# Kernel optimization log

Measured on AMD Instinct MI355X. Metric: run time of the kernel, lower is better.

The kernel has to match this reference:

```python
import jax, jax.numpy as jnp
import numpy as np
from jax import lax

B, C, H, W = 4, 256, 64, 64
R = 4  # reduction
BN_EPS = 1e-5


def setup_inputs() -> dict:
    key = jax.random.key(0)
    ks = jax.random.split(key, 18)
    n = jax.random.normal
    return {
        "x_self": n(ks[0], (B, C, H, W), jnp.float32),
        "x_other": n(ks[1], (B, C, H, W), jnp.float32),
        "q_w": n(ks[2], (C, C), jnp.float32) * 0.05,      # self_q 1x1 conv
        "q_b": n(ks[3], (C,), jnp.float32) * 0.05,
        "kv_w": n(ks[4], (2 * C, C), jnp.float32) * 0.05,  # other_kv 1x1 conv
        "kv_b": n(ks[5], (2 * C,), jnp.float32) * 0.05,
        "g1_w": n(ks[6], (C // R, C), jnp.float32) * 0.05,  # gate conv1
        "g1_b": n(ks[7], (C // R,), jnp.float32) * 0.05,
        "g2_w": n(ks[8], (1, C // R), jnp.float32) * 0.05,  # gate conv2
        "g2_b": n(ks[9], (1,), jnp.float32) * 0.05,
        "dw_w": n(ks[10], (C, 1, 3, 3), jnp.float32) * 0.1,  # depthwise 3x3
        "dw_b": n(ks[11], (C,), jnp.float32) * 0.05,
        "bn_g": jnp.ones((C,), jnp.float32),
        "bn_b": jnp.zeros((C,), jnp.float32),
        "bn_m": n(ks[12], (C,), jnp.float32) * 0.05,
        "bn_v": jax.random.uniform(ks[13], (C,), jnp.float32, 0.5, 1.5),
        "out_w": n(ks[14], (C, C), jnp.float32) * 0.05,
        "out_b": n(ks[15], (C,), jnp.float32) * 0.05,
    }


def _conv1x1(x, w, b):
    return jnp.einsum('bchw,oc->bohw', x, w) + b[None, :, None, None]


def reference(x_self, x_other, q_w, q_b, kv_w, kv_b, g1_w, g1_b, g2_w, g2_b,
              dw_w, dw_b, bn_g, bn_b, bn_m, bn_v, out_w, out_b):
    # local branch: depthwise 3x3 conv -> BatchNorm (eval stats) -> SiLU
    y = lax.conv_general_dilated(
        x_self, dw_w, (1, 1), 'SAME',
        feature_group_count=C,
        dimension_numbers=('NCHW', 'OIHW', 'NCHW')) + dw_b[None, :, None, None]
    scale = (bn_g / jnp.sqrt(bn_v + BN_EPS))[None, :, None, None]
    y = (y - bn_m[None, :, None, None]) * scale + bn_b[None, :, None, None]
    local_feat = y * jax.nn.sigmoid(y)  # SiLU

    # cross attention over HW tokens
    q = _conv1x1(x_self, q_w, q_b).reshape(B, C, H * W)
    kv = _conv1x1(x_other, kv_w, kv_b)
    k = kv[:, :C].reshape(B, C, H * W)
    v = kv[:, C:].reshape(B, C, H * W)
    attn = jnp.einsum('bcn,bcm->bnm', q, k) / jnp.sqrt(jnp.float32(C))  # [B,HW,HW]
    attn = jax.nn.softmax(attn, axis=-1)
    attn_out = jnp.einsum('bnm,bcm->bcn', attn, v).reshape(B, C, H, W)

    # channel-squeeze gate on x_self -> scalar per sample
    p = jnp.mean(x_self, axis=(2, 3))                 # [B,C] global avg pool
    g = jax.nn.relu(p @ g1_w.T + g1_b)                # [B,C//R]
    g = jax.nn.sigmoid(g @ g2_w.T + g2_b)             # [B,1]
    gate = g[:, :, None, None]

    fused = local_feat + gate * attn_out
    return _conv1x1(fused, out_w, out_b)
```

## Files before the change

kernel.cpp:

```cpp
#include <hip/hip_runtime.h>
#include <stdint.h>

#define BB 4
#define CC 256
#define HH 64
#define WWD 64
#define NN 4096
#define LOG2E 1.4426950408889634f

typedef __attribute__((ext_vector_type(8))) short short8;
typedef __attribute__((ext_vector_type(4))) float f32x4;
typedef __attribute__((ext_vector_type(16))) float f32x16;
typedef __attribute__((ext_vector_type(4))) unsigned short us4;
typedef unsigned long long ull;

__device__ __forceinline__ unsigned short f2bf(float f) {
  unsigned int u = __float_as_uint(f);
  u += 0x7fffu + ((u >> 16) & 1u);
  return (unsigned short)(u >> 16);
}
__device__ __forceinline__ float bf2f(unsigned short h) {
  return __uint_as_float(((unsigned int)h) << 16);
}
__device__ __forceinline__ short8 ld8(const unsigned short* p) {
  return *reinterpret_cast<const short8*>(p);
}
__device__ __forceinline__ unsigned char f2fp8(float v) {
  return (unsigned char)__builtin_amdgcn_cvt_pk_fp8_f32(v, v, 0, false);
}
__device__ __forceinline__ int rowmap(int reg, int h) {
  return (reg & 3) + 8 * (reg >> 2) + 4 * h;
}
__device__ __forceinline__ void gll16(const void* g, void* l) {
  __builtin_amdgcn_global_load_lds(
      (const __attribute__((address_space(1))) unsigned int*)g,
      (__attribute__((address_space(3))) unsigned int*)l, 16, 0, 0);
}

__global__ __launch_bounds__(256, 2) void k_pre(
    const float* __restrict__ xs, const float* __restrict__ xo,
    const float* __restrict__ dww, const float* __restrict__ dwb,
    const float* __restrict__ bng, const float* __restrict__ bnb,
    const float* __restrict__ bnm, const float* __restrict__ bnv,
    const float* __restrict__ qw, const float* __restrict__ kvw,
    const float* __restrict__ ow, unsigned short* __restrict__ XtS,
    unsigned short* __restrict__ XtO, unsigned short* __restrict__ localT,
    float* __restrict__ psumA, unsigned short* __restrict__ Wb) {
  __shared__ float rb3[3][64][67];
  __shared__ unsigned short sb[64][67];
  int tid = threadIdx.x;
  if (blockIdx.z == 8) {
    int i = (blockIdx.x * 64 + blockIdx.y) * 1024 + tid * 4;
    const float* src;
    if (i < 65536) src = qw + i;
    else if (i < 196608) src = kvw + (i - 65536);
    else src = ow + (i - 196608);
    f32x4 v = *reinterpret_cast<const f32x4*>(src);
    us4 r;
#pragma unroll
    for (int j = 0; j < 4; ++j) r[j] = f2bf(v[j]);
    *reinterpret_cast<us4*>(Wb + i) = r;
    return;
  }
  int c0 = blockIdx.x * 64, h = blockIdx.y;
  int b = blockIdx.z >> 1, which = blockIdx.z & 1;
  const float* src = which ? xo : xs;
  int wq = tid >> 6, w = tid & 63;
  int dlo = which ? 1 : 0, dhi = which ? 1 : 2;
  for (int d = dlo; d <= dhi; ++d) {
    int hh = h + d - 1;
    bool ok = (hh >= 0 && hh < HH);
#pragma unroll
    for (int p = 0; p < 4; ++p) {
      int idx = p * 256 + tid;
      int cl = idx >> 4, ws4 = (idx & 15) * 4;
      f32x4 v = {};
      if (ok)
        v = *reinterpret_cast<const f32x4*>(
            &src[(((size_t)(b * CC + c0 + cl)) * HH + hh) * WWD + ws4]);
#pragma unroll
      for (int j = 0; j < 4; ++j) rb3[d][cl][ws4 + 1 + j] = v[j];
    }
    if (tid < 64) { rb3[d][tid][0] = 0.f; rb3[d][tid][65] = 0.f; }
  }
  __syncthreads();
  unsigned short* dst = which ? XtO : XtS;
  int n0 = h * 64, cb = (tid & 15) * 4;
#pragma unroll
  for (int i = 0; i < 4; ++i) {
    int wl = i * 16 + (tid >> 4);
    us4 r;
#pragma unroll
    for (int j = 0; j < 4; ++j) r[j] = f2bf(rb3[1][cb + j][wl + 1]);
    *reinterpret_cast<us4*>(&dst[((size_t)b * NN + n0 + wl) * CC + c0 + cb]) = r;
  }
  if (which) return;
  if (tid < 64) {
    float s = 0.f;
    for (int ww = 0; ww < 64; ++ww) s += rb3[1][tid][ww + 1];
    psumA[((size_t)(b * 64 + h)) * CC + c0 + tid] = s;
  }
  for (int p = 0; p < 16; ++p) {
    int cl = p * 4 + wq, c = c0 + cl;
    float acc = 0.f;
#pragma unroll
    for (int di = 0; di < 3; ++di)
#pragma unroll
      for (int dj = 0; dj < 3; ++dj)
        acc = fmaf(rb3[di][cl][w + dj], dww[c * 9 + di * 3 + dj], acc);
    float y = acc + dwb[c];
    float sc = bng[c] * rsqrtf(bnv[c] + 1e-5f);
    float v = (y - bnm[c]) * sc + bnb[c];
    sb[cl][w] = f2bf(v / (1.f + __expf(-v)));
  }
  __syncthreads();
#pragma unroll
  for (int i = 0; i < 4; ++i) {
    int wl = i * 16 + (tid >> 4);
    us4 r;
#pragma unroll
    for (int j = 0; j < 4; ++j) r[j] = sb[cb + j][wl];
    *reinterpret_cast<us4*>(&localT[((size_t)b * NN + h * WWD + wl) * CC + c0 + cb]) = r;
  }
}

__global__ __launch_bounds__(256, 4) void k_qkv(
    const unsigned short* __restrict__ XtS, const unsigned short* __restrict__ XtO,
    const unsigned short* __restrict__ Wb, const float* __restrict__ qb,
    const float* __restrict__ kvb, const float* __restrict__ psumA,
    const float* __restrict__ g1w, const float* __restrict__ g1b,
    const float* __restrict__ g2w, const float* __restrict__ g2b,
    unsigned char* __restrict__ Qt8, unsigned char* __restrict__ Kt8,
    unsigned char* __restrict__ Vv8, float* __restrict__ gate) {
  __shared__ unsigned short Xs[64][264];
  int tid = threadIdx.x;
  int id = blockIdx.y;
  if (id == 3) {
    if (blockIdx.x != 0 || blockIdx.z != 0) return;
    float* mf = (float*)&Xs[0][0];
    float* hpf = mf + 1024;
    int c = tid;
    for (int b4 = 0; b4 < 4; ++b4) {
      float s = 0.f;
      for (int hh = 0; hh < 64; ++hh) s += psumA[((size_t)(b4 * 64 + hh)) * CC + c];
      mf[b4 * 256 + c] = s * (1.f / 4096.f);
    }
    __syncthreads();
    for (int b4 = 0; b4 < 4; ++b4) {
      int j = tid >> 2, cq = tid & 3;
      float s = 0.f;
      for (int cc = cq * 64; cc < cq * 64 + 64; ++cc)
        s = fmaf(mf[b4 * 256 + cc], g1w[j * CC + cc], s);
      hpf[j * 5 + cq] = s;
      __syncthreads();
      if (tid < 64) {
        float hh = fmaxf(hpf[tid * 5] + hpf[tid * 5 + 1] + hpf[tid * 5 + 2] +
                             hpf[tid * 5 + 3] + g1b[tid], 0.f);
        float t = hh * g2w[tid];
        for (int off = 32; off; off >>= 1) t += __shfl_down(t, off, 64);
        if (tid == 0) gate[b4] = 1.f / (1.f + expf(-(t + g2b[0])));
      }
      __syncthreads();
    }
    return;
  }
  int n0 = blockIdx.x * 64, b = blockIdx.z;
  const unsigned short* Xt = (id == 0) ? XtS : XtO;
  const unsigned short* W = Wb + id * 65536;
  int wave = tid >> 6, lane = tid & 63, l31 = lane & 31, h = lane >> 5;
#pragma unroll
  for (int p = 0; p < 8; ++p) {
    int r = p * 8 + (tid >> 5), c = (tid & 31) * 8;
    *reinterpret_cast<uint4*>(&Xs[r][c]) =
        *reinterpret_cast<const uint4*>(Xt + ((size_t)b * NN + n0 + r) * CC + c);
  }
  __syncthreads();
  int o0 = wave * 64;
  f32x16 acc[4] = {};
  if (id < 2) {
#pragma unroll
    for (int t = 0; t < 16; ++t) {
      short8 a0 = ld8(&Xs[l31][t * 16 + h * 8]);
      short8 a1 = ld8(&Xs[32 + l31][t * 16 + h * 8]);
      short8 b0 = ld8(W + (size_t)(o0 + l31) * CC + t * 16 + h * 8);
      short8 b1 = ld8(W + (size_t)(o0 + 32 + l31) * CC + t * 16 + h * 8);
      acc[0] = __builtin_amdgcn_mfma_f32_32x32x16_bf16(a0, b0, acc[0], 0, 0, 0);
      acc[1] = __builtin_amdgcn_mfma_f32_32x32x16_bf16(a0, b1, acc[1], 0, 0, 0);
      acc[2] = __builtin_amdgcn_mfma_f32_32x32x16_bf16(a1, b0, acc[2], 0, 0, 0);
      acc[3] = __builtin_amdgcn_mfma_f32_32x32x16_bf16(a1, b1, acc[3], 0, 0, 0);
    }
    const float* bias = id ? kvb : qb;
    unsigned char* Out8 = id ? Kt8 : Qt8;
    __syncthreads();
    unsigned char (*T8)[264] = reinterpret_cast<unsigned char(*)[264]>(&Xs[0][0]);
#pragma unroll
    for (int nt = 0; nt < 2; ++nt)
#pragma unroll
      for (int ot = 0; ot < 2; ++ot) {
        int o = o0 + ot * 32 + l31;
        float bv = bias[o];
#pragma unroll
        for (int reg = 0; reg < 16; ++reg) {
          int nl = nt * 32 + rowmap(reg, h);
          T8[nl][o] = f2fp8((acc[nt * 2 + ot][reg] + bv) * 0.25f);
        }
      }
    __syncthreads();
#pragma unroll
    for (int p = 0; p < 4; ++p) {
      int idx = p * 256 + tid, row = idx >> 4, cc = (idx & 15) * 16;
      int s = (id == 1) ? ((row & 31) << 3) : 0;
      ull a0 = *reinterpret_cast<const ull*>(&T8[row][cc ^ s]);
      ull a1 = *reinterpret_cast<const ull*>(&T8[row][(cc + 8) ^ s]);
      uint4 u;
      u.x = (unsigned)a0; u.y = (unsigned)(a0 >> 32);
      u.z = (unsigned)a1; u.w = (unsigned)(a1 >> 32);
      *reinterpret_cast<uint4*>(Out8 + ((size_t)b * NN + n0 + row) * CC + cc) = u;
    }
  } else {
#pragma unroll
    for (int t = 0; t < 16; ++t) {
      short8 a0 = ld8(W + (size_t)(o0 + l31) * CC + t * 16 + h * 8);
      short8 a1 = ld8(W + (size_t)(o0 + 32 + l31) * CC + t * 16 + h * 8);
      short8 b0 = ld8(&Xs[l31][t * 16 + h * 8]);
      short8 b1 = ld8(&Xs[32 + l31][t * 16 + h * 8]);
      acc[0] = __builtin_amdgcn_mfma_f32_32x32x16_bf16(a0, b0, acc[0], 0, 0, 0);
      acc[1] = __builtin_amdgcn_mfma_f32_32x32x16_bf16(a0, b1, acc[1], 0, 0, 0);
      acc[2] = __builtin_amdgcn_mfma_f32_32x32x16_bf16(a1, b0, acc[2], 0, 0, 0);
      acc[3] = __builtin_amdgcn_mfma_f32_32x32x16_bf16(a1, b1, acc[3], 0, 0, 0);
    }
    __syncthreads();
    unsigned char (*V8)[72] = reinterpret_cast<unsigned char(*)[72]>(&Xs[0][0]);
#pragma unroll
    for (int ot = 0; ot < 2; ++ot)
#pragma unroll
      for (int nt = 0; nt < 2; ++nt)
#pragma unroll
        for (int reg = 0; reg < 16; ++reg) {
          int o = o0 + ot * 32 + rowmap(reg, h);
          int nl = nt * 32 + l31;
          V8[o][nl] = f2fp8(acc[ot * 2 + nt][reg] + kvb[CC + o]);
        }
    __syncthreads();
#pragma unroll
    for (int p = 0; p < 4; ++p) {
      int idx = p * 256 + tid, o = idx >> 2, mm = (idx & 3) * 16;
      int s = (o & 7) << 3;
      ull a0 = *reinterpret_cast<const ull*>(&V8[o][mm ^ s]);
      ull a1 = *reinterpret_cast<const ull*>(&V8[o][(mm + 8) ^ s]);
      uint4 u;
      u.x = (unsigned)a0; u.y = (unsigned)(a0 >> 32);
      u.z = (unsigned)a1; u.w = (unsigned)(a1 >> 32);
      *reinterpret_cast<uint4*>(Vv8 + ((size_t)b * CC + o) * NN + n0 + mm) = u;
    }
  }
}

__global__ __launch_bounds__(256, 3) void k_flash8(
    const unsigned char* __restrict__ Qt8, const unsigned char* __restrict__ Kt8,
    const unsigned char* __restrict__ Vv8, const unsigned short* __restrict__ localT,
    const float* __restrict__ gate, unsigned short* __restrict__ Opart16,
    float* __restrict__ Lpart, unsigned short* __restrict__ fusedT) {
  __shared__ unsigned char Ks8[64][256];
  __shared__ unsigned char Vs8[2][256][64];
  __shared__ unsigned char Ps8[64][72];
  __shared__ float lred[2][64];
  int b = blockIdx.x & 3, n0 = (blockIdx.x >> 2) * 64;
  int sp = blockIdx.y, nsp = gridDim.y;
  int tid = threadIdx.x, wave = tid >> 6, lane = tid & 63, l31 = lane & 31, h = lane >> 5;
  int rw = wave & 1, cw = wave >> 1;
  int wbase = tid & ~63;
  const unsigned char* qp = Qt8 + ((size_t)b * NN + n0 + rw * 32 + l31) * CC + h * 8;
  long qf[16];
#pragma unroll
  for (int t = 0; t < 16; ++t) qf[t] = *reinterpret_cast<const long*>(qp + t * 16);
  f32x16 O[4] = {};
  float lsum = 0.f;
  int m_lo = (64 * sp) / nsp, m_hi = (64 * (sp + 1)) / nsp;
  const unsigned char* Kbase = Kt8 + (size_t)b * NN * CC;
  const unsigned char* Vbase = Vv8 + (size_t)b * CC * NN;
  {
    const unsigned char* Kg = Kbase + (size_t)(m_lo * 64) * CC;
    const unsigned char* Vg = Vbase + m_lo * 64;
    unsigned char* vdst = &Vs8[m_lo & 1][0][0];
#pragma unroll
    for (int p = 0; p < 4; ++p) {
      int idx = p * 256 + tid;
      int c = idx >> 2, mm = (idx & 3) * 16;
      gll16(Vg + (size_t)c * NN + mm, vdst + (p * 256 + wbase) * 16);
      gll16(Kg + (size_t)idx * 16, &Ks8[0][0] + (p * 256 + wbase) * 16);
    }
  }
  const unsigned char* Krow = &Ks8[cw * 32 + l31][0];
  int ksw = l31 << 3;
  int vsw = (l31 & 7) << 3;
  for (int mt = m_lo; mt < m_hi; ++mt) {
    asm volatile("s_waitcnt vmcnt(0)" ::: "memory");
    __builtin_amdgcn_s_barrier();
    __builtin_amdgcn_sched_barrier(0);
    {
      int mn = (mt + 1 < m_hi) ? mt + 1 : mt;
      const unsigned char* Vg = Vbase + mn * 64;
      unsigned char* vdst = &Vs8[(mt + 1) & 1][0][0];
#pragma unroll
      for (int p = 0; p < 4; ++p) {
        int idx = p * 256 + tid;
        int c = idx >> 2, mm = (idx & 3) * 16;
        gll16(Vg + (size_t)c * NN + mm, vdst + (p * 256 + wbase) * 16);
      }
    }
    __builtin_amdgcn_sched_barrier(0);
    f32x16 S = {};
#pragma unroll
    for (int t = 0; t < 16; ++t) {
      long kf = *reinterpret_cast<const long*>(Krow + ((t * 16 + h * 8) ^ ksw));
      S = __builtin_amdgcn_mfma_f32_32x32x16_fp8_fp8(kf, qf[t], S, 0, 0, 0);
    }
#pragma unroll
    for (int r = 0; r < 4; ++r) {
      float p0 = __builtin_exp2f(S[4 * r + 0] * LOG2E);
      float p1 = __builtin_exp2f(S[4 * r + 1] * LOG2E);
      float p2 = __builtin_exp2f(S[4 * r + 2] * LOG2E);
      float p3 = __builtin_exp2f(S[4 * r + 3] * LOG2E);
      lsum += (p0 + p1) + (p2 + p3);
      unsigned u = __builtin_amdgcn_cvt_pk_fp8_f32(p0, p1, 0, false);
      u = __builtin_amdgcn_cvt_pk_fp8_f32(p2, p3, u, true);
      *reinterpret_cast<unsigned*>(&Ps8[rw * 32 + l31][cw * 32 + 8 * r + 4 * h]) = u;
    }
    asm volatile("s_waitcnt lgkmcnt(0)" ::: "memory");
    __builtin_amdgcn_s_barrier();
    __builtin_amdgcn_sched_barrier(0);
    {
      int mn = (mt + 1 < m_hi) ? mt + 1 : mt;
      const unsigned char* Kg = Kbase + (size_t)(mn * 64) * CC;
#pragma unroll
      for (int p = 0; p < 4; ++p)
        gll16(Kg + (size_t)(p * 256 + tid) * 16, &Ks8[0][0] + (p * 256 + wbase) * 16);
    }
    __builtin_amdgcn_sched_barrier(0);
    const unsigned char (*Vc)[64] = Vs8[mt & 1];
#pragma unroll
    for (int t = 0; t < 4; ++t) {
      long pf = *reinterpret_cast<const long*>(&Ps8[rw * 32 + l31][t * 16 + h * 8]);
#pragma unroll
      for (int ct = 0; ct < 4; ++ct) {
        long vf = *reinterpret_cast<const long*>(
            &Vc[cw * 128 + ct * 32 + l31][(t * 16 + h * 8) ^ vsw]);
        O[ct] = __builtin_amdgcn_mfma_f32_32x32x16_fp8_fp8(pf, vf, O[ct], 0, 0, 0);
      }
    }
  }
  asm volatile("s_waitcnt vmcnt(0)" ::: "memory");
  lsum += __shfl_xor(lsum, 32, 64);
  __syncthreads();
  if (h == 0) lred[cw][rw * 32 + l31] = lsum;
  __syncthreads();
  size_t obase2 = (size_t)(b * nsp + sp) * NN;
  if (nsp == 1) {
    float* ltot = reinterpret_cast<float*>(&Ps8[0][0]);
    if (tid < 64) ltot[tid] = lred[0][tid] + lred[1][tid];
    __syncthreads();
    float gv = gate[b];
    float inv[16];
#pragma unroll
    for (int reg = 0; reg < 16; ++reg)
      inv[reg] = gv / ltot[rw * 32 + rowmap(reg, h)];
#pragma unroll
    for (int ct = 0; ct < 4; ++ct)
#pragma unroll
      for (int reg = 0; reg < 16; ++reg) {
        int n = n0 + rw * 32 + rowmap(reg, h);
        int c = cw * 128 + ct * 32 + l31;
        size_t idx = ((size_t)b * NN + n) * CC + c;
        fusedT[idx] = f2bf(bf2f(localT[idx]) + O[ct][reg] * inv[reg]);
      }
  } else {
    if (tid < 64) Lpart[obase2 + n0 + tid] = lred[0][tid] + lred[1][tid];
#pragma unroll
    for (int ct = 0; ct < 4; ++ct)
#pragma unroll
      for (int reg = 0; reg < 16; ++reg) {
        int n = n0 + rw * 32 + rowmap(reg, h);
        int c = cw * 128 + ct * 32 + l31;
        Opart16[(obase2 + n) * CC + c] = f2bf(O[ct][reg]);
      }
  }
}

__global__ __launch_bounds__(256, 4) void k_out(
    const unsigned short* __restrict__ W, const float* __restrict__ ob,
    const float* __restrict__ gate, const unsigned short* __restrict__ localT,
    const unsigned short* __restrict__ Opart16, const float* __restrict__ Lpart,
    const unsigned short* __restrict__ fusedT, float* __restrict__ out, int nsp) {
  __shared__ unsigned short Xs[64][264];
  int n0 = blockIdx.x * 64, o0 = blockIdx.y * 128, b = blockIdx.z;
  int tid = threadIdx.x, wave = tid >> 6, lane = tid & 63, l31 = lane & 31, h = lane >> 5;
  if (Opart16) {
    float gv = gate[b];
#pragma unroll
    for (int p = 0; p < 8; ++p) {
      int r = p * 8 + (tid >> 5), cc = (tid & 31) * 8;
      int n = n0 + r;
      float lsum = 0.f;
      for (int sp = 0; sp < nsp; ++sp) lsum += Lpart[(size_t)(b * nsp + sp) * NN + n];
      float g = gv / lsum;
      float ov[8] = {};
      for (int sp = 0; sp < nsp; ++sp) {
        short8 x = ld8(Opart16 + ((size_t)(b * nsp + sp) * NN + n) * CC + cc);
#pragma unroll
        for (int j = 0; j < 8; ++j) ov[j] += bf2f(((unsigned short*)&x)[j]);
      }
      const unsigned short* lp = localT + ((size_t)b * NN + n) * CC + cc;
      short8 lv = ld8(lp);
      us4 r0, r1;
#pragma unroll
      for (int j = 0; j < 4; ++j) {
        r0[j] = f2bf(bf2f(((unsigned short*)&lv)[j]) + ov[j] * g);
        r1[j] = f2bf(bf2f(((unsigned short*)&lv)[j + 4]) + ov[j + 4] * g);
      }
      *reinterpret_cast<us4*>(&Xs[r][cc]) = r0;
      *reinterpret_cast<us4*>(&Xs[r][cc + 4]) = r1;
    }
  } else {
#pragma unroll
    for (int p = 0; p < 8; ++p) {
      int r = p * 8 + (tid >> 5), c = (tid & 31) * 8;
      *reinterpret_cast<uint4*>(&Xs[r][c]) =
          *reinterpret_cast<const uint4*>(fusedT + ((size_t)b * NN + n0 + r) * CC + c);
    }
  }
  int obase = o0 + wave * 32;
  short8 af[16];
#pragma unroll
  for (int t = 0; t < 16; ++t) af[t] = ld8(W + (size_t)(obase + l31) * CC + t * 16 + h * 8);
  __syncthreads();
  f32x16 acc[2] = {};
#pragma unroll
  for (int t = 0; t < 16; ++t) {
    short8 b0 = ld8(&Xs[l31][t * 16 + h * 8]);
    short8 b1 = ld8(&Xs[32 + l31][t * 16 + h * 8]);
    acc[0] = __builtin_amdgcn_mfma_f32_32x32x16_bf16(af[t], b0, acc[0], 0, 0, 0);
    acc[1] = __builtin_amdgcn_mfma_f32_32x32x16_bf16(af[t], b1, acc[1], 0, 0, 0);
  }
#pragma unroll
  for (int nt = 0; nt < 2; ++nt)
#pragma unroll
    for (int reg = 0; reg < 16; ++reg) {
      int o = obase + rowmap(reg, h);
      int n = n0 + nt * 32 + l31;
      out[((size_t)b * CC + o) * NN + n] = acc[nt][reg] + ob[o];
    }
}

extern "C" void kernel_launch(void* const* d_in, const int* in_sizes, int n_in,
                              void* d_out, int out_size, void* d_ws, size_t ws_size,
                              hipStream_t stream) {
  const float* xs  = (const float*)d_in[0];
  const float* xo  = (const float*)d_in[1];
  const float* qw  = (const float*)d_in[2];
  const float* qb  = (const float*)d_in[3];
  const float* kvw = (const float*)d_in[4];
  const float* kvb = (const float*)d_in[5];
  const float* g1w = (const float*)d_in[6];
  const float* g1b = (const float*)d_in[7];
  const float* g2w = (const float*)d_in[8];
  const float* g2b = (const float*)d_in[9];
  const float* dww = (const float*)d_in[10];
  const float* dwb = (const float*)d_in[11];
  const float* bng = (const float*)d_in[12];
  const float* bnb = (const float*)d_in[13];
  const float* bnm = (const float*)d_in[14];
  const float* bnv = (const float*)d_in[15];
  const float* ow  = (const float*)d_in[16];
  const float* ob  = (const float*)d_in[17];
  float* out = (float*)d_out;
  char* ws = (char*)d_ws;

  const size_t SZ  = (size_t)BB * NN * CC * 2;
  const size_t SZ8 = (size_t)BB * NN * CC;
  unsigned short* XtS    = (unsigned short*)(ws);
  unsigned short* XtO    = (unsigned short*)(ws + SZ);
  unsigned short* localT = (unsigned short*)(ws + 2 * SZ);
  unsigned char*  Qt8    = (unsigned char*)(ws + 3 * SZ);
  unsigned char*  Kt8    = (unsigned char*)(ws + 3 * SZ + SZ8);
  unsigned char*  Vv8    = (unsigned char*)(ws + 3 * SZ + 2 * SZ8);
  unsigned short* Wb     = (unsigned short*)(ws + 3 * SZ + 3 * SZ8);
  float* psumA = (float*)(ws + 3 * SZ + 3 * SZ8 + 524288);
  float* gate  = (float*)(ws + 3 * SZ + 3 * SZ8 + 524288 + 262144);
  size_t tail  = 3 * SZ + 3 * SZ8 + 524288 + 262144 + 4096;
  float* Lpart = (float*)(ws + tail);
  unsigned short* Opart16 = (unsigned short*)(ws + tail + 262144);
  unsigned short* fusedT = XtS;

  size_t base = tail + 262144;
  int S = 1;
  if (ws_size >= base + 3ull * SZ) S = 3;
  else if (ws_size >= base + 2ull * SZ) S = 2;

  k_pre<<<dim3(4, 64, 9), 256, 0, stream>>>(xs, xo, dww, dwb, bng, bnb, bnm, bnv,
                                            qw, kvw, ow, XtS, XtO, localT, psumA, Wb);
  k_qkv<<<dim3(64, 4, 4), 256, 0, stream>>>(XtS, XtO, Wb, qb, kvb, psumA,
                                            g1w, g1b, g2w, g2b, Qt8, Kt8, Vv8, gate);
  k_flash8<<<dim3(256, S), 256, 0, stream>>>(Qt8, Kt8, Vv8, localT, gate, Opart16,
                                             Lpart, fusedT);
  k_out<<<dim3(64, 2, 4), 256, 0, stream>>>(Wb + 196608, ob, gate, localT,
                                            S > 1 ? Opart16 : nullptr, Lpart, fusedT,
                                            out, S);
}
```

Before: 258.9 us.

## Split QK MFMA chain, reuse XtO for partial output, retune V swizzle and priority

Splits the QK^T accumulation into two independent MFMA chains to shorten the dependency chain, and raises wave priority around the MFMA loops with s_setprio. Changes the V tile XOR swizzle to use row pairs, both where V is written and where it is read in the flash kernel. Stores the first split's partial output in the now-dead XtO buffer, so less extra workspace is needed and three splits become possible with smaller workspace. The risk is a mismatch between the swizzle on the write side and the read side, and extra register pressure from the second accumulator.

```diff
diff --git a/kernel.cpp b/kernel.cpp
--- a/kernel.cpp
+++ b/kernel.cpp
@@ -245,7 +245,7 @@
 #pragma unroll
     for (int p = 0; p < 4; ++p) {
       int idx = p * 256 + tid, o = idx >> 2, mm = (idx & 3) * 16;
-      int s = (o & 7) << 3;
+      int s = ((o >> 1) & 7) << 3;
       ull a0 = *reinterpret_cast<const ull*>(&V8[o][mm ^ s]);
       ull a1 = *reinterpret_cast<const ull*>(&V8[o][(mm + 8) ^ s]);
       uint4 u;
@@ -259,7 +259,8 @@
 __global__ __launch_bounds__(256, 3) void k_flash8(
     const unsigned char* __restrict__ Qt8, const unsigned char* __restrict__ Kt8,
     const unsigned char* __restrict__ Vv8, const unsigned short* __restrict__ localT,
-    const float* __restrict__ gate, unsigned short* __restrict__ Opart16,
+    const float* __restrict__ gate, unsigned short* __restrict__ OpartA,
+    unsigned short* __restrict__ OpartB,
     float* __restrict__ Lpart, unsigned short* __restrict__ fusedT) {
   __shared__ unsigned char Ks8[64][256];
   __shared__ unsigned char Vs8[2][256][64];
@@ -275,7 +276,7 @@
 #pragma unroll
   for (int t = 0; t < 16; ++t) qf[t] = *reinterpret_cast<const long*>(qp + t * 16);
   f32x16 O[4] = {};
-  float lsum = 0.f;
+  float lsumA = 0.f, lsumB = 0.f;
   int m_lo = (64 * sp) / nsp, m_hi = (64 * (sp + 1)) / nsp;
   const unsigned char* Kbase = Kt8 + (size_t)b * NN * CC;
   const unsigned char* Vbase = Vv8 + (size_t)b * CC * NN;
@@ -293,7 +294,7 @@
   }
   const unsigned char* Krow = &Ks8[cw * 32 + l31][0];
   int ksw = l31 << 3;
-  int vsw = (l31 & 7) << 3;
+  int vsw = ((l31 >> 1) & 7) << 3;
   for (int mt = m_lo; mt < m_hi; ++mt) {
     asm volatile("s_waitcnt vmcnt(0)" ::: "memory");
     __builtin_amdgcn_s_barrier();
@@ -310,19 +311,24 @@
       }
     }
     __builtin_amdgcn_sched_barrier(0);
-    f32x16 S = {};
-#pragma unroll
-    for (int t = 0; t < 16; ++t) {
-      long kf = *reinterpret_cast<const long*>(Krow + ((t * 16 + h * 8) ^ ksw));
-      S = __builtin_amdgcn_mfma_f32_32x32x16_fp8_fp8(kf, qf[t], S, 0, 0, 0);
-    }
+    f32x16 Sa = {}, Sb = {};
+    __builtin_amdgcn_s_setprio(1);
+#pragma unroll
+    for (int t = 0; t < 8; ++t) {
+      long kfa = *reinterpret_cast<const long*>(Krow + ((t * 16 + h * 8) ^ ksw));
+      long kfb = *reinterpret_cast<const long*>(Krow + (((t + 8) * 16 + h * 8) ^ ksw));
+      Sa = __builtin_amdgcn_mfma_f32_32x32x16_fp8_fp8(kfa, qf[t], Sa, 0, 0, 0);
+      Sb = __builtin_amdgcn_mfma_f32_32x32x16_fp8_fp8(kfb, qf[t + 8], Sb, 0, 0, 0);
+    }
+    __builtin_amdgcn_s_setprio(0);
 #pragma unroll
     for (int r = 0; r < 4; ++r) {
-      float p0 = __builtin_exp2f(S[4 * r + 0] * LOG2E);
-      float p1 = __builtin_exp2f(S[4 * r + 1] * LOG2E);
-      float p2 = __builtin_exp2f(S[4 * r + 2] * LOG2E);
-      float p3 = __builtin_exp2f(S[4 * r + 3] * LOG2E);
-      lsum += (p0 + p1) + (p2 + p3);
+      float p0 = __builtin_exp2f((Sa[4 * r + 0] + Sb[4 * r + 0]) * LOG2E);
+      float p1 = __builtin_exp2f((Sa[4 * r + 1] + Sb[4 * r + 1]) * LOG2E);
+      float p2 = __builtin_exp2f((Sa[4 * r + 2] + Sb[4 * r + 2]) * LOG2E);
+      float p3 = __builtin_exp2f((Sa[4 * r + 3] + Sb[4 * r + 3]) * LOG2E);
+      lsumA += p0 + p1;
+      lsumB += p2 + p3;
       unsigned u = __builtin_amdgcn_cvt_pk_fp8_f32(p0, p1, 0, false);
       u = __builtin_amdgcn_cvt_pk_fp8_f32(p2, p3, u, true);
       *reinterpret_cast<unsigned*>(&Ps8[rw * 32 + l31][cw * 32 + 8 * r + 4 * h]) = u;
@@ -339,6 +345,7 @@
     }
     __builtin_amdgcn_sched_barrier(0);
     const unsigned char (*Vc)[64] = Vs8[mt & 1];
+    __builtin_amdgcn_s_setprio(1);
 #pragma unroll
     for (int t = 0; t < 4; ++t) {
       long pf = *reinterpret_cast<const long*>(&Ps8[rw * 32 + l31][t * 16 + h * 8]);
@@ -349,13 +356,14 @@
         O[ct] = __builtin_amdgcn_mfma_f32_32x32x16_fp8_fp8(pf, vf, O[ct], 0, 0, 0);
       }
     }
+    __builtin_amdgcn_s_setprio(0);
   }
   asm volatile("s_waitcnt vmcnt(0)" ::: "memory");
+  float lsum = lsumA + lsumB;
   lsum += __shfl_xor(lsum, 32, 64);
   __syncthreads();
   if (h == 0) lred[cw][rw * 32 + l31] = lsum;
   __syncthreads();
-  size_t obase2 = (size_t)(b * nsp + sp) * NN;
   if (nsp == 1) {
     float* ltot = reinterpret_cast<float*>(&Ps8[0][0]);
     if (tid < 64) ltot[tid] = lred[0][tid] + lred[1][tid];
@@ -375,14 +383,18 @@
         fusedT[idx] = f2bf(bf2f(localT[idx]) + O[ct][reg] * inv[reg]);
       }
   } else {
-    if (tid < 64) Lpart[obase2 + n0 + tid] = lred[0][tid] + lred[1][tid];
+    if (tid < 64) Lpart[(size_t)(b * nsp + sp) * NN + n0 + tid] = lred[0][tid] + lred[1][tid];
+    unsigned short* Op;
+    size_t slab;
+    if (sp == 0) { Op = OpartA; slab = (size_t)b * NN; }
+    else { Op = OpartB; slab = (size_t)(b * (nsp - 1) + (sp - 1)) * NN; }
 #pragma unroll
     for (int ct = 0; ct < 4; ++ct)
 #pragma unroll
       for (int reg = 0; reg < 16; ++reg) {
         int n = n0 + rw * 32 + rowmap(reg, h);
         int c = cw * 128 + ct * 32 + l31;
-        Opart16[(obase2 + n) * CC + c] = f2bf(O[ct][reg]);
+        Op[(slab + n) * CC + c] = f2bf(O[ct][reg]);
       }
   }
 }
@@ -390,12 +402,13 @@
 __global__ __launch_bounds__(256, 4) void k_out(
     const unsigned short* __restrict__ W, const float* __restrict__ ob,
     const float* __restrict__ gate, const unsigned short* __restrict__ localT,
-    const unsigned short* __restrict__ Opart16, const float* __restrict__ Lpart,
+    const unsigned short* __restrict__ OpartA, const unsigned short* __restrict__ OpartB,
+    const float* __restrict__ Lpart,
     const unsigned short* __restrict__ fusedT, float* __restrict__ out, int nsp) {
   __shared__ unsigned short Xs[64][264];
   int n0 = blockIdx.x * 64, o0 = blockIdx.y * 128, b = blockIdx.z;
   int tid = threadIdx.x, wave = tid >> 6, lane = tid & 63, l31 = lane & 31, h = lane >> 5;
-  if (Opart16) {
+  if (nsp > 1) {
     float gv = gate[b];
 #pragma unroll
     for (int p = 0; p < 8; ++p) {
@@ -406,7 +419,11 @@
       float g = gv / lsum;
       float ov[8] = {};
       for (int sp = 0; sp < nsp; ++sp) {
-        short8 x = ld8(Opart16 + ((size_t)(b * nsp + sp) * NN + n) * CC + cc);
+        const unsigned short* Op;
+        size_t slab;
+        if (sp == 0) { Op = OpartA; slab = (size_t)b * NN; }
+        else { Op = OpartB; slab = (size_t)(b * (nsp - 1) + (sp - 1)) * NN; }
+        short8 x = ld8(Op + (slab + n) * CC + cc);
 #pragma unroll
         for (int j = 0; j < 8; ++j) ov[j] += bf2f(((unsigned short*)&x)[j]);
       }
@@ -489,21 +506,21 @@
   float* gate  = (float*)(ws + 3 * SZ + 3 * SZ8 + 524288 + 262144);
   size_t tail  = 3 * SZ + 3 * SZ8 + 524288 + 262144 + 4096;
   float* Lpart = (float*)(ws + tail);
-  unsigned short* Opart16 = (unsigned short*)(ws + tail + 262144);
+  unsigned short* OpartA = XtO;
+  unsigned short* OpartB = (unsigned short*)(ws + tail + 262144);
   unsigned short* fusedT = XtS;
 
   size_t base = tail + 262144;
   int S = 1;
-  if (ws_size >= base + 3ull * SZ) S = 3;
-  else if (ws_size >= base + 2ull * SZ) S = 2;
+  if (ws_size >= base + 2ull * SZ) S = 3;
+  else if (ws_size >= base + 1ull * SZ) S = 2;
 
   k_pre<<<dim3(4, 64, 9), 256, 0, stream>>>(xs, xo, dww, dwb, bng, bnb, bnm, bnv,
                                             qw, kvw, ow, XtS, XtO, localT, psumA, Wb);
   k_qkv<<<dim3(64, 4, 4), 256, 0, stream>>>(XtS, XtO, Wb, qb, kvb, psumA,
                                             g1w, g1b, g2w, g2b, Qt8, Kt8, Vv8, gate);
-  k_flash8<<<dim3(256, S), 256, 0, stream>>>(Qt8, Kt8, Vv8, localT, gate, Opart16,
-                                             Lpart, fusedT);
+  k_flash8<<<dim3(256, S), 256, 0, stream>>>(Qt8, Kt8, Vv8, localT, gate, OpartA,
+                                             OpartB, Lpart, fusedT);
   k_out<<<dim3(64, 2, 4), 256, 0, stream>>>(Wb + 196608, ob, gate, localT,
-                                            S > 1 ? Opart16 : nullptr, Lpart, fusedT,
-                                            out, S);
-}
+                                            OpartA, OpartB, Lpart, fusedT, out, S);
+}
```

Result: slower. 292.0 us (+12.8%).
